# Optimization experiments

Hardware: AMD Instinct MI355X
Metric: run time of the kernel (lower is better)

## Reference

```python
import jax, jax.numpy as jnp
from jax import lax
import numpy as np

B, L, E, H, R, V = 64, 512, 256, 256, 50, 20000
NEG = 1e10  # seq_max_pool mask constant


def _conv1d(x, w, b):
    # x: (B, L, Cin) -> (B, L, Cout); kernel 3, 'same' padding (pad=1)
    y = lax.conv_general_dilated(x.transpose(0, 2, 1), w, (1,), [(1, 1)],
                                 dimension_numbers=('NCH', 'OIH', 'NCH'))
    return y.transpose(0, 2, 1) + b


def _lstm_step(x, h, c, W_ih, W_hh, b_ih, b_hh):
    # single-step LSTM, PyTorch gate order (i, f, g, o)
    gates = x @ W_ih.T + b_ih + h @ W_hh.T + b_hh
    i, f, g, o = jnp.split(gates, 4, axis=-1)
    c = jax.nn.sigmoid(f) * c + jax.nn.sigmoid(i) * jnp.tanh(g)
    h = jax.nn.sigmoid(o) * jnp.tanh(c)
    return h, c


def _attention(q, ctx, W_attn, b_attn):
    # Luong attention (IBM seq2seq style). q: (B,E), ctx: (B,L,E)
    scores = jnp.einsum('be,ble->bl', q, ctx)
    attn = jax.nn.softmax(scores, axis=-1)
    mix = jnp.einsum('bl,ble->be', attn, ctx)
    return jnp.tanh(jnp.concatenate([mix, q], axis=-1) @ W_attn.T + b_attn)


def setup_inputs() -> dict:
    key = jax.random.key(0)
    ks = jax.random.split(key, 25)
    s = 0.05
    return {
        'encoder_o': jax.random.normal(ks[0], (B, L, E), jnp.float32),
        'h0': jax.random.normal(ks[1], (B, H), jnp.float32),
        'c0': jax.random.normal(ks[2], (B, H), jnp.float32),
        'sos_emb': jax.random.normal(ks[3], (E,), jnp.float32) * s,
        'rel_emb': jax.random.normal(ks[4], (R, E), jnp.float32) * s,
        'W_ih': jax.random.normal(ks[5], (4 * H, E), jnp.float32) * s,
        'W_hh': jax.random.normal(ks[6], (4 * H, H), jnp.float32) * s,
        'b_ih': jax.random.normal(ks[7], (4 * H,), jnp.float32) * s,
        'b_hh': jax.random.normal(ks[8], (4 * H,), jnp.float32) * s,
        'W_attn': jax.random.normal(ks[9], (E, 2 * E), jnp.float32) * s,
        'b_attn': jax.random.normal(ks[10], (E,), jnp.float32) * s,
        'conv_rel_w': jax.random.normal(ks[11], (E, 2 * H, 3), jnp.float32) * s,
        'conv_rel_b': jax.random.normal(ks[12], (E,), jnp.float32) * s,
        'conv_ent_w': jax.random.normal(ks[13], (E, 2 * H, 3), jnp.float32) * s,
        'conv_ent_b': jax.random.normal(ks[14], (E,), jnp.float32) * s,
        'W_rel': jax.random.normal(ks[15], (R, E), jnp.float32) * s,
        'b_rel': jax.random.normal(ks[16], (R,), jnp.float32) * s,
        'w_e1': jax.random.normal(ks[17], (E,), jnp.float32) * s,
        'b_e1': jax.random.normal(ks[18], (1,), jnp.float32) * s,
        'w_e2': jax.random.normal(ks[19], (E,), jnp.float32) * s,
        'b_e2': jax.random.normal(ks[20], (1,), jnp.float32) * s,
        'T': jax.random.randint(ks[21], (B, L), 0, V),
        'R_in': jax.random.randint(ks[22], (B,), 0, R),
        'S_K1': jax.random.randint(ks[23], (B,), 0, L),
        'S_K2': jax.random.randint(ks[24], (B,), 0, L),
    }


def reference(encoder_o, h0, c0, sos_emb, rel_emb, W_ih, W_hh, b_ih, b_hh,
              W_attn, b_attn, conv_rel_w, conv_rel_b, conv_ent_w, conv_ent_b,
              W_rel, b_rel, w_e1, b_e1, w_e2, b_e2, T, R_in, S_K1, S_K2):
    # train_forward, order=('subject','predicate','object') -> sos2ent, ent2rel, rel2ent
    # dropout is identity (eval mode)
    mask = (T > 0).astype(encoder_o.dtype)[..., None]  # (B,L,1)
    bidx = jnp.arange(B)

    def step(inp, h, c, enc, conv_w, conv_b):
        # forward_step: one LSTM step + attention over enc
        h, c = _lstm_step(inp, h, c, W_ih, W_hh, b_ih, b_hh)
        out = _attention(h, enc, W_attn, b_attn)  # (B,E)
        # seq_and_vec + permute + conv1d + permute
        cat = jnp.concatenate([enc, jnp.broadcast_to(out[:, None, :], enc.shape)], axis=-1)
        new_enc = _conv1d(cat, conv_w, conv_b)  # (B,L,E)
        a = jax.nn.gelu(new_enc, approximate=False)
        return a, new_enc, h, c

    # step 1: sos -> entity heads
    a, enc1, h, c = step(jnp.broadcast_to(sos_emb, (B, E)), h0, c0, encoder_o,
                         conv_ent_w, conv_ent_b)
    t1e1 = a @ w_e1 + b_e1  # (B,L)
    t1e2 = a @ w_e2 + b_e2

    # step 2: gathered entity span vectors -> relation logits (masked max-pool)
    inp = enc1[bidx, S_K1] + enc1[bidx, S_K2]  # seq_gather + sum, (B,E)
    a, enc2, h, c = step(inp, h, c, enc1, conv_rel_w, conv_rel_b)
    logits = a @ W_rel.T + b_rel  # (B,L,R)
    t2rel = jnp.max(logits - (1.0 - mask) * NEG, axis=1)  # seq_max_pool -> (B,R)

    # step 3: relation embedding -> entity heads
    a, enc3, h, c = step(rel_emb[R_in], h, c, enc2, conv_ent_w, conv_ent_b)
    t3e1 = a @ w_e1 + b_e1
    t3e2 = a @ w_e2 + b_e2

    return (t1e1, t1e2, t2rel, t3e1, t3e2)
```

## Files before the change

### kernel.cpp

```cpp
#include <hip/hip_runtime.h>
#include <math.h>

#define B_ 64
#define L_ 512
#define E_ 256
#define H_ 256
#define R_ 50
#define NEG_ 1.0e10f

typedef __bf16 bf16x8 __attribute__((ext_vector_type(8)));
typedef float f32x4 __attribute__((ext_vector_type(4)));

__device__ __forceinline__ float sigmoidf_(float x) { return 1.0f / (1.0f + expf(-x)); }
__device__ __forceinline__ float geluf_(float x) { return 0.5f * x * (1.0f + erff(x * 0.7071067811865476f)); }
__device__ __forceinline__ unsigned short f2bf(float x) {
    unsigned u = __float_as_uint(x);
    return (unsigned short)((u + 0x7fffu + ((u >> 16) & 1u)) >> 16);
}
__device__ __forceinline__ float bf2f(unsigned u) { return __uint_as_float(u << 16); }

__global__ void k_packs(const float* __restrict__ encoder_o, unsigned short* __restrict__ encBF0,
                        const float* __restrict__ conv_ent_w, const float* __restrict__ conv_rel_w,
                        unsigned short* __restrict__ bpE, unsigned short* __restrict__ bpR,
                        const float* __restrict__ W_rel, unsigned short* __restrict__ wpR,
                        float* __restrict__ wpkE, float* __restrict__ wpkR,
                        const float* __restrict__ W_attn, float* __restrict__ WTat) {
    const int blk = blockIdx.x, t = threadIdx.x;
    if (blk < 8192) {
        size_t idx = (size_t)blk * 256 + t;
        float4 v = *(const float4*)&encoder_o[idx * 4];
        uint2 p;
        p.x = (unsigned)f2bf(v.x) | ((unsigned)f2bf(v.y) << 16);
        p.y = (unsigned)f2bf(v.z) | ((unsigned)f2bf(v.w) << 16);
        *(uint2*)&encBF0[idx * 4] = p;
    } else if (blk < 8384) {
        const float* w = (blk < 8288) ? conv_ent_w : conv_rel_w;
        unsigned short* bp = (blk < 8288) ? bpE : bpR;
        int idx = (blk - ((blk < 8288) ? 8192 : 8288)) * 256 + t;
        int l = idx & 63, kc = (idx >> 6) % 24, of = idx / (24 * 64);
        int o = of * 16 + (l & 15);
        int k = kc >> 3;
        int cb = ((kc & 7) << 5) + ((l >> 4) << 3);
        unsigned short v[8];
#pragma unroll
        for (int j = 0; j < 8; ++j) v[j] = f2bf(w[(size_t)o * 1536 + (size_t)(cb + j) * 3 + k]);
        unsigned int* dst = (unsigned int*)&bp[(size_t)idx * 8];
#pragma unroll
        for (int j = 0; j < 4; ++j) dst[j] = (unsigned int)v[2 * j] | ((unsigned int)v[2 * j + 1] << 16);
    } else if (blk < 8392) {
        int idx = (blk - 8384) * 256 + t;
        int l = idx & 63, kc = (idx >> 6) & 7, of = idx / (8 * 64);
        int r = of * 16 + (l & 15);
        int k = kc * 32 + ((l >> 4) << 3);
        unsigned short v[8];
#pragma unroll
        for (int j = 0; j < 8; ++j) v[j] = (r < R_) ? f2bf(W_rel[(size_t)r * E_ + k + j]) : 0;
        unsigned int* dst = (unsigned int*)&wpR[(size_t)idx * 8];
#pragma unroll
        for (int j = 0; j < 4; ++j) dst[j] = (unsigned int)v[2 * j] | ((unsigned int)v[2 * j + 1] << 16);
    } else if (blk < 8904) {
        const float* w = (blk < 8648) ? conv_ent_w : conv_rel_w;
        float* wpk = (blk < 8648) ? wpkE : wpkR;
        int idx = (blk - ((blk < 8648) ? 8392 : 8648)) * 256 + t;
        int o = idx >> 8, c = idx & 255;
        const float* p = &w[(size_t)o * 1536 + 768 + c * 3];
        float w0 = p[0], w1 = p[1], w2 = p[2];
        wpk[c * 256 + o] = w0;
        wpk[65536 + c * 256 + o] = w0 + w1 + w2;
        wpk[131072 + c * 256 + o] = w2;
    } else {
        int idx = (blk - 8904) * 256 + t;
        int o = idx >> 9, k = idx & 511;
        WTat[k * 256 + o] = W_attn[idx];
    }
}

template <int MODE>
__global__ __launch_bounds__(256) void k_lstm_gemm(
    const float* __restrict__ xsrc_f, const unsigned short* __restrict__ encg,
    const int* __restrict__ i1, const int* __restrict__ i2, const int* __restrict__ rin,
    const float* __restrict__ hprev,
    const float* __restrict__ W_ih, const float* __restrict__ W_hh,
    float* __restrict__ gates,
    const float* __restrict__ pmax, float* __restrict__ t2rel) {
    const int g0 = blockIdx.x * 64;
    const int half = blockIdx.y, z = blockIdx.z;
    const int t = threadIdx.x, tx = t & 15, ty = t >> 4;
    __shared__ float Xs[64][68];
    __shared__ float Wt[64][68];
    const float* Wsrc = half ? W_hh : W_ih;
    float acc[4][4] = {{0.f}};
    for (int kb = z * 128; kb < z * 128 + 128; kb += 64) {
        __syncthreads();
#pragma unroll
        for (int i = 0; i < 4; ++i) {
            int idx = i * 256 + t;
            int row = idx >> 4, kk = (idx & 15) << 2;
            float4 xv;
            if (half) {
                xv = *(const float4*)&hprev[row * 256 + kb + kk];
            } else if (MODE == 0) {
                xv = *(const float4*)&xsrc_f[kb + kk];
            } else if (MODE == 2) {
                xv = *(const float4*)&xsrc_f[(size_t)rin[row] * 256 + kb + kk];
            } else {
                const unsigned short* p1 = &encg[((size_t)row * L_ + i1[row]) * E_ + kb + kk];
                const unsigned short* p2 = &encg[((size_t)row * L_ + i2[row]) * E_ + kb + kk];
                uint2 a = *(const uint2*)p1, b2 = *(const uint2*)p2;
                xv.x = bf2f(a.x & 0xffffu) + bf2f(b2.x & 0xffffu);
                xv.y = bf2f(a.x >> 16) + bf2f(b2.x >> 16);
                xv.z = bf2f(a.y & 0xffffu) + bf2f(b2.y & 0xffffu);
                xv.w = bf2f(a.y >> 16) + bf2f(b2.y >> 16);
            }
            *(float4*)&Xs[row][kk] = xv;
            *(float4*)&Wt[row][kk] = *(const float4*)&Wsrc[(size_t)(g0 + row) * 256 + kb + kk];
        }
        __syncthreads();
#pragma unroll
        for (int kk = 0; kk < 64; kk += 4) {
            float4 xv[4], wv[4];
#pragma unroll
            for (int i = 0; i < 4; ++i) xv[i] = *(const float4*)&Xs[ty * 4 + i][kk];
#pragma unroll
            for (int j = 0; j < 4; ++j) wv[j] = *(const float4*)&Wt[tx * 4 + j][kk];
#pragma unroll
            for (int i = 0; i < 4; ++i)
#pragma unroll
                for (int j = 0; j < 4; ++j)
                    acc[i][j] += xv[i].x * wv[j].x + xv[i].y * wv[j].y + xv[i].z * wv[j].z + xv[i].w * wv[j].w;
        }
    }
    const int seg = half * 2 + z;
#pragma unroll
    for (int i = 0; i < 4; ++i)
#pragma unroll
        for (int j = 0; j < 4; ++j)
            gates[(size_t)seg * 65536 + (size_t)(ty * 4 + i) * 1024 + g0 + tx * 4 + j] = acc[i][j];

    if (MODE == 2 && blockIdx.x == 0 && half == 0 && z == 0) {
        for (int i = t; i < B_ * 64; i += 256) {
            int b = i >> 6, r = i & 63;
            if (r < R_) {
                float m = -3.0e38f;
#pragma unroll
                for (int ch = 0; ch < 8; ++ch) m = fmaxf(m, pmax[((size_t)b * 8 + ch) * 64 + r]);
                t2rel[b * R_ + r] = m;
            }
        }
    }
}

__global__ __launch_bounds__(256) void k_attn_part(
    const float* __restrict__ gates, const float* __restrict__ b_ih, const float* __restrict__ b_hh,
    const float* __restrict__ c_in, float* __restrict__ c_out, float* __restrict__ h_out,
    const unsigned short* __restrict__ encbf,
    float* __restrict__ mixp, float* __restrict__ stats) {
    int b = blockIdx.y, ch = blockIdx.x, t = threadIdx.x;
    __shared__ float hs[E_];
    __shared__ float scp[64][4];
    __shared__ float sc[64];
    {
        size_t ba = (size_t)b * 1024;
        float g4[4];
#pragma unroll
        for (int g = 0; g < 4; ++g) {
            float acc = b_ih[g * 256 + t] + b_hh[g * 256 + t];
#pragma unroll
            for (int seg = 0; seg < 4; ++seg) acc += gates[(size_t)seg * 65536 + ba + g * 256 + t];
            g4[g] = acc;
        }
        float c = sigmoidf_(g4[1]) * c_in[b * H_ + t] + sigmoidf_(g4[0]) * tanhf(g4[2]);
        float hv = sigmoidf_(g4[3]) * tanhf(c);
        hs[t] = hv;
        if (ch == 0) { h_out[b * H_ + t] = hv; c_out[b * H_ + t] = c; }
    }
    __syncthreads();
    {
        int row = t >> 2, es = t & 3;
        const uint4* p = (const uint4*)&encbf[((size_t)b * L_ + ch * 64 + row) * E_ + es * 64];
        float acc = 0.f;
#pragma unroll
        for (int k = 0; k < 8; ++k) {
            uint4 q = p[k];
            int e0 = es * 64 + k * 8;
            acc += bf2f(q.x & 0xffffu) * hs[e0] + bf2f(q.x >> 16) * hs[e0 + 1]
                 + bf2f(q.y & 0xffffu) * hs[e0 + 2] + bf2f(q.y >> 16) * hs[e0 + 3]
                 + bf2f(q.z & 0xffffu) * hs[e0 + 4] + bf2f(q.z >> 16) * hs[e0 + 5]
                 + bf2f(q.w & 0xffffu) * hs[e0 + 6] + bf2f(q.w >> 16) * hs[e0 + 7];
        }
        scp[row][es] = acc;
    }
    __syncthreads();
    if (t < 64) {
        float v = scp[t][0] + scp[t][1] + scp[t][2] + scp[t][3];
        float m = v;
#pragma unroll
        for (int off = 32; off; off >>= 1) m = fmaxf(m, __shfl_xor(m, off));
        float ev = expf(v - m);
        float s = ev;
#pragma unroll
        for (int off = 32; off; off >>= 1) s += __shfl_xor(s, off);
        sc[t] = ev;
        if (t == 0) {
            stats[((size_t)b * 8 + ch) * 2] = m;
            stats[((size_t)b * 8 + ch) * 2 + 1] = s;
        }
    }
    __syncthreads();
    float acc = 0.f;
    const unsigned short* base = &encbf[((size_t)b * L_ + ch * 64) * E_ + t];
#pragma unroll 8
    for (int l = 0; l < 64; ++l) acc += sc[l] * bf2f((unsigned)base[(size_t)l * E_]);
    mixp[((size_t)b * 8 + ch) * E_ + t] = acc;
}

__global__ __launch_bounds__(256) void k_post1(
    const float* __restrict__ mixp, const float* __restrict__ stats,
    const float* __restrict__ h, const float* __restrict__ WT_attn,
    const float* __restrict__ b_attn, float* __restrict__ aout) {
    int b = blockIdx.x, oc = blockIdx.y, t = threadIdx.x;
    __shared__ float cat[512];
    __shared__ float red[16][16][4];
    {
        float M = -3.0e38f;
#pragma unroll
        for (int i = 0; i < 8; ++i) M = fmaxf(M, stats[(b * 8 + i) * 2]);
        float denom = 0.f, mixv = 0.f;
#pragma unroll
        for (int i = 0; i < 8; ++i) {
            float w = expf(stats[(b * 8 + i) * 2] - M);
            denom += stats[(b * 8 + i) * 2 + 1] * w;
            mixv += mixp[((size_t)b * 8 + i) * E_ + t] * w;
        }
        cat[t] = mixv / denom;
        cat[256 + t] = h[b * H_ + t];
    }
    __syncthreads();
    int ocol = t & 15, ks = t >> 4;
    int o4 = oc * 64 + ocol * 4;
    float a0 = 0.f, a1 = 0.f, a2 = 0.f, a3 = 0.f;
    const float* wp = &WT_attn[(size_t)(ks * 32) * 256 + o4];
#pragma unroll 8
    for (int k = 0; k < 32; ++k) {
        float4 w = *(const float4*)&wp[(size_t)k * 256];
        float cv = cat[ks * 32 + k];
        a0 += cv * w.x; a1 += cv * w.y; a2 += cv * w.z; a3 += cv * w.w;
    }
    red[ks][ocol][0] = a0; red[ks][ocol][1] = a1; red[ks][ocol][2] = a2; red[ks][ocol][3] = a3;
    __syncthreads();
    if (t < 64) {
        int oc2 = t >> 2, j = t & 3;
        float s = 0.f;
#pragma unroll
        for (int k2 = 0; k2 < 16; ++k2) s += red[k2][oc2][j];
        int o = oc * 64 + t;
        aout[b * E_ + o] = tanhf(s + b_attn[o]);
    }
}

__global__ __launch_bounds__(256) void k_post2(
    const float* __restrict__ aout, const float* __restrict__ wpk,
    float* __restrict__ cr0, float* __restrict__ fullv, float* __restrict__ cr2) {
    int b = blockIdx.x, m = blockIdx.y, t = threadIdx.x;
    __shared__ float os[256];
    __shared__ float red[4][64][4];
    os[t] = aout[b * E_ + t];
    __syncthreads();
    int ocol = t & 63, cs = t >> 6;
    int o4 = ocol * 4;
    const float* wp = &wpk[(size_t)m * 65536 + (size_t)(cs * 64) * 256 + o4];
    float a0 = 0.f, a1 = 0.f, a2 = 0.f, a3 = 0.f;
#pragma unroll 8
    for (int c = 0; c < 64; ++c) {
        float4 w = *(const float4*)&wp[(size_t)c * 256];
        float v = os[cs * 64 + c];
        a0 += v * w.x; a1 += v * w.y; a2 += v * w.z; a3 += v * w.w;
    }
    red[cs][ocol][0] = a0; red[cs][ocol][1] = a1; red[cs][ocol][2] = a2; red[cs][ocol][3] = a3;
    __syncthreads();
    int oc2 = t >> 2, j = t & 3;
    float s = red[0][oc2][j] + red[1][oc2][j] + red[2][oc2][j] + red[3][oc2][j];
    float* dst = (m == 0) ? cr0 : (m == 1) ? fullv : cr2;
    dst[b * E_ + t] = s;
}

template <bool FUSE_HEADS, bool WRITE_OUT, bool FUSE_REL>
__global__ __launch_bounds__(512, 6) void k_conv_mfma(
    const unsigned short* __restrict__ encbf, const unsigned short* __restrict__ bp,
    const float* __restrict__ bias, const float* __restrict__ fullv,
    const float* __restrict__ cr0, const float* __restrict__ cr2,
    unsigned short* __restrict__ enc_out,
    const float* __restrict__ w_e1, const float* __restrict__ b_e1,
    const float* __restrict__ w_e2, const float* __restrict__ b_e2,
    float* __restrict__ o1, float* __restrict__ o2,
    const unsigned short* __restrict__ wprel, const float* __restrict__ b_rel,
    const int* __restrict__ T, float* __restrict__ pmax) {
    const int b = blockIdx.y, l0 = blockIdx.x * 64;
    const int t = threadIdx.x, lane = t & 63, wid = t >> 6;
    __shared__ unsigned short As[66 * 256];
    __shared__ float hsum[2][FUSE_HEADS ? 8 : 1][FUSE_HEADS ? 64 : 1];
    __shared__ float pm[FUSE_REL ? 8 : 1][2][16];
    __shared__ int Tm[FUSE_REL ? 64 : 1];

    if (FUSE_REL && t < 64) Tm[t] = T[b * L_ + l0 + t];

    for (int u = t; u < 66 * 32; u += 512) {
        int row = u >> 5, cu = u & 31;
        int l = l0 - 1 + row;
        uint4 v = {0u, 0u, 0u, 0u};
        if (l >= 0 && l < L_) v = *(const uint4*)&encbf[((size_t)b * L_ + l) * E_ + cu * 8];
        *(uint4*)&As[row * 256 + ((cu ^ (row & 7)) << 3)] = v;
    }
    __syncthreads();

    const int wo2 = wid * 2;
    f32x4 zero = {0.f, 0.f, 0.f, 0.f};
    f32x4 acc[4][2];
#pragma unroll
    for (int i = 0; i < 4; ++i) { acc[i][0] = zero; acc[i][1] = zero; }
    const int arow = lane & 15, agrp = lane >> 4;
    const unsigned short* bp0 = &bp[((size_t)wo2 * 24 * 64 + lane) * 8];
    const unsigned short* bp1 = &bp[((size_t)(wo2 + 1) * 24 * 64 + lane) * 8];

#pragma unroll 4
    for (int kc = 0; kc < 24; ++kc) {
        const int k = kc >> 3;
        const int g = ((kc & 7) << 2) + agrp;
        bf16x8 b0 = *(const bf16x8*)&bp0[(size_t)kc * 512];
        bf16x8 b1 = *(const bf16x8*)&bp1[(size_t)kc * 512];
#pragma unroll
        for (int mi = 0; mi < 4; ++mi) {
            int r = mi * 16 + arow + k;
            bf16x8 a = *(const bf16x8*)&As[r * 256 + ((g ^ (r & 7)) << 3)];
            acc[mi][0] = __builtin_amdgcn_mfma_f32_16x16x32_bf16(a, b0, acc[mi][0], 0, 0, 0);
            acc[mi][1] = __builtin_amdgcn_mfma_f32_16x16x32_bf16(a, b1, acc[mi][1], 0, 0, 0);
        }
    }

    float biasv[2], c0v[2], c2v[2], we1v[2], we2v[2];
#pragma unroll
    for (int ni = 0; ni < 2; ++ni) {
        int o = (wo2 + ni) * 16 + (lane & 15);
        biasv[ni] = bias[o] + fullv[b * E_ + o];
        c0v[ni] = cr0[b * E_ + o];
        c2v[ni] = cr2[b * E_ + o];
        if (FUSE_HEADS) { we1v[ni] = w_e1[o]; we2v[ni] = w_e2[o]; }
    }
    __syncthreads();

#pragma unroll
    for (int mi = 0; mi < 4; ++mi) {
#pragma unroll
        for (int r = 0; r < 4; ++r) {
            int lloc = mi * 16 + agrp * 4 + r;
            int lrow = l0 + lloc;
            float p1 = 0.f, p2 = 0.f;
#pragma unroll
            for (int ni = 0; ni < 2; ++ni) {
                int o = (wo2 + ni) * 16 + (lane & 15);
                float vv = acc[mi][ni][r] + biasv[ni];
                if (lrow == 0) vv -= c0v[ni];
                if (lrow == L_ - 1) vv -= c2v[ni];
                if (WRITE_OUT || FUSE_REL) {
                    int idx = FUSE_REL ? (lloc * 256 + ((((o >> 3) ^ (lloc & 7))) << 3) + (o & 7))
                                       : (lloc * 256 + o);
                    As[idx] = f2bf(vv);
                }
                if (FUSE_HEADS) {
                    float gv = geluf_(vv);
                    p1 += gv * we1v[ni];
                    p2 += gv * we2v[ni];
                }
            }
            if (FUSE_HEADS) {
#pragma unroll
                for (int off = 1; off < 16; off <<= 1) {
                    p1 += __shfl_xor(p1, off);
                    p2 += __shfl_xor(p2, off);
                }
                if ((lane & 15) == 0) {
                    hsum[0][wid][lloc] = p1;
                    hsum[1][wid][lloc] = p2;
                }
            }
        }
    }
    __syncthreads();

    if (WRITE_OUT) {
        for (int u = t; u < 64 * 32; u += 512) {
            int row = u >> 5, cu = u & 31;
            int src = FUSE_REL ? (row * 256 + ((cu ^ (row & 7)) << 3)) : (row * 256 + cu * 8);
            uint4 q = *(const uint4*)&As[src];
            *(uint4*)&enc_out[((size_t)b * L_ + l0 + row) * E_ + cu * 8] = q;
            if (FUSE_REL) {
                unsigned qa[4] = {q.x, q.y, q.z, q.w};
#pragma unroll
                for (int j = 0; j < 4; ++j) {
                    unsigned lo = f2bf(geluf_(bf2f(qa[j] & 0xffffu)));
                    unsigned hi = f2bf(geluf_(bf2f(qa[j] >> 16)));
                    qa[j] = lo | (hi << 16);
                }
                uint4 gq = {qa[0], qa[1], qa[2], qa[3]};
                *(uint4*)&As[src] = gq;
            }
        }
    }
    if (FUSE_HEADS && t < 128) {
        int hh = t >> 6, row = t & 63;
        float s = 0.f;
#pragma unroll
        for (int w = 0; w < 8; ++w) s += hsum[hh][w][row];
        float* dst = hh ? o2 : o1;
        const float* bb = hh ? b_e2 : b_e1;
        dst[(size_t)b * L_ + l0 + row] = s + bb[0];
    }
    if (FUSE_REL) {
        __syncthreads();
        const int mi = wid & 3, njp = wid >> 2;
        f32x4 accr[2] = {zero, zero};
        const int ar = mi * 16 + arow;
#pragma unroll 2
        for (int kc = 0; kc < 8; ++kc) {
            int g = (kc << 2) + agrp;
            bf16x8 av = *(const bf16x8*)&As[ar * 256 + ((g ^ (ar & 7)) << 3)];
#pragma unroll
            for (int q = 0; q < 2; ++q) {
                int nj = njp * 2 + q;
                bf16x8 bv = *(const bf16x8*)&wprel[(((size_t)nj * 8 + kc) * 64 + lane) * 8];
                accr[q] = __builtin_amdgcn_mfma_f32_16x16x32_bf16(av, bv, accr[q], 0, 0, 0);
            }
        }
#pragma unroll
        for (int q = 0; q < 2; ++q) {
            int nj = njp * 2 + q;
            int rr = nj * 16 + (lane & 15);
            float brel = (rr < R_) ? b_rel[rr] : 0.f;
            float v = -3.0e38f;
#pragma unroll
            for (int rg = 0; rg < 4; ++rg) {
                int lloc = mi * 16 + agrp * 4 + rg;
                float pen = (Tm[lloc] > 0) ? 0.f : NEG_;
                v = fmaxf(v, accr[q][rg] + brel - pen);
            }
            v = fmaxf(v, __shfl_xor(v, 16));
            v = fmaxf(v, __shfl_xor(v, 32));
            if (lane < 16) pm[wid][q][lane] = v;
        }
        __syncthreads();
        if (t < 64) {
            int nj = t >> 4, rl = t & 15;
            int q = nj & 1, wb = (nj >> 1) * 4;
            float m = fmaxf(fmaxf(pm[wb][q][rl], pm[wb + 1][q][rl]),
                            fmaxf(pm[wb + 2][q][rl], pm[wb + 3][q][rl]));
            pmax[((size_t)b * 8 + blockIdx.x) * 64 + t] = m;
        }
    }
}

extern "C" void kernel_launch(void* const* d_in, const int* in_sizes, int n_in,
                              void* d_out, int out_size, void* d_ws, size_t ws_size,
                              hipStream_t stream) {
    const float* encoder_o = (const float*)d_in[0];
    const float* h0 = (const float*)d_in[1];
    const float* c0 = (const float*)d_in[2];
    const float* sos_emb = (const float*)d_in[3];
    const float* rel_emb = (const float*)d_in[4];
    const float* W_ih = (const float*)d_in[5];
    const float* W_hh = (const float*)d_in[6];
    const float* b_ih = (const float*)d_in[7];
    const float* b_hh = (const float*)d_in[8];
    const float* W_attn = (const float*)d_in[9];
    const float* b_attn = (const float*)d_in[10];
    const float* conv_rel_w = (const float*)d_in[11];
    const float* conv_rel_b = (const float*)d_in[12];
    const float* conv_ent_w = (const float*)d_in[13];
    const float* conv_ent_b = (const float*)d_in[14];
    const float* W_rel = (const float*)d_in[15];
    const float* b_rel = (const float*)d_in[16];
    const float* w_e1 = (const float*)d_in[17];
    const float* b_e1 = (const float*)d_in[18];
    const float* w_e2 = (const float*)d_in[19];
    const float* b_e2 = (const float*)d_in[20];
    const int* T = (const int*)d_in[21];
    const int* R_in = (const int*)d_in[22];
    const int* S_K1 = (const int*)d_in[23];
    const int* S_K2 = (const int*)d_in[24];

    float* out = (float*)d_out;
    float* t1e1 = out;
    float* t1e2 = out + 32768;
    float* t2rel = out + 65536;
    float* t3e1 = out + 68736;
    float* t3e2 = out + 101504;

    float* ws = (float*)d_ws;
    size_t off = 0;
    unsigned short* encBF0 = (unsigned short*)(ws + off); off += (size_t)B_ * L_ * E_ / 2;
    unsigned short* encA = (unsigned short*)(ws + off); off += (size_t)B_ * L_ * E_ / 2;
    unsigned short* encB = (unsigned short*)(ws + off); off += (size_t)B_ * L_ * E_ / 2;
    float* gates = ws + off; off += 4 * 65536;
    float* hbuf = ws + off; off += B_ * H_;
    float* cb1 = ws + off; off += B_ * H_;
    float* cb2 = ws + off; off += B_ * H_;
    float* cb3 = ws + off; off += B_ * H_;
    float* mixp = ws + off; off += (size_t)B_ * 8 * E_;
    float* stats = ws + off; off += B_ * 8 * 2;
    float* aoutb = ws + off; off += B_ * E_;
    float* fullv = ws + off; off += B_ * E_;
    float* cr0 = ws + off; off += B_ * E_;
    float* cr2 = ws + off; off += B_ * E_;
    float* pmax = ws + off; off += B_ * 8 * 64;
    float* wpkE = ws + off; off += 3 * 65536;
    float* wpkR = ws + off; off += 3 * 65536;
    float* WTat = ws + off; off += 131072;
    unsigned short* bpE = (unsigned short*)(ws + off); off += 16 * 24 * 64 * 8 / 2;
    unsigned short* bpR = (unsigned short*)(ws + off); off += 16 * 24 * 64 * 8 / 2;
    unsigned short* wpR = (unsigned short*)(ws + off); off += 4 * 8 * 64 * 8 / 2;

    dim3 convGrid(8, B_);
    dim3 attnGrid(8, B_);
    dim3 lstmGrid(16, 2, 2);
    dim3 p1Grid(B_, 4);
    dim3 p2Grid(B_, 3);

    k_packs<<<9416, 256, 0, stream>>>(encoder_o, encBF0, conv_ent_w, conv_rel_w,
                                      bpE, bpR, W_rel, wpR, wpkE, wpkR, W_attn, WTat);

    k_lstm_gemm<0><<<lstmGrid, 256, 0, stream>>>(sos_emb, nullptr, nullptr, nullptr, nullptr,
                                                 h0, W_ih, W_hh, gates, nullptr, nullptr);
    k_attn_part<<<attnGrid, 256, 0, stream>>>(gates, b_ih, b_hh, c0, cb1, hbuf, encBF0, mixp, stats);
    k_post1<<<p1Grid, 256, 0, stream>>>(mixp, stats, hbuf, WTat, b_attn, aoutb);
    k_post2<<<p2Grid, 256, 0, stream>>>(aoutb, wpkE, cr0, fullv, cr2);
    k_conv_mfma<true, true, false><<<convGrid, 512, 0, stream>>>(
        encBF0, bpE, conv_ent_b, fullv, cr0, cr2, encA,
        w_e1, b_e1, w_e2, b_e2, t1e1, t1e2, nullptr, nullptr, nullptr, nullptr);

    k_lstm_gemm<1><<<lstmGrid, 256, 0, stream>>>(nullptr, encA, S_K1, S_K2, nullptr,
                                                 hbuf, W_ih, W_hh, gates, nullptr, nullptr);
    k_attn_part<<<attnGrid, 256, 0, stream>>>(gates, b_ih, b_hh, cb1, cb2, hbuf, encA, mixp, stats);
    k_post1<<<p1Grid, 256, 0, stream>>>(mixp, stats, hbuf, WTat, b_attn, aoutb);
    k_post2<<<p2Grid, 256, 0, stream>>>(aoutb, wpkR, cr0, fullv, cr2);
    k_conv_mfma<false, true, true><<<convGrid, 512, 0, stream>>>(
        encA, bpR, conv_rel_b, fullv, cr0, cr2, encB,
        nullptr, nullptr, nullptr, nullptr, nullptr, nullptr, wpR, b_rel, T, pmax);

    k_lstm_gemm<2><<<lstmGrid, 256, 0, stream>>>(rel_emb, nullptr, nullptr, nullptr, R_in,
                                                 hbuf, W_ih, W_hh, gates, pmax, t2rel);
    k_attn_part<<<attnGrid, 256, 0, stream>>>(gates, b_ih, b_hh, cb2, cb3, hbuf, encB, mixp, stats);
    k_post1<<<p1Grid, 256, 0, stream>>>(mixp, stats, hbuf, WTat, b_attn, aoutb);
    k_post2<<<p2Grid, 256, 0, stream>>>(aoutb, wpkE, cr0, fullv, cr2);
    k_conv_mfma<true, false, false><<<convGrid, 512, 0, stream>>>(
        encB, bpE, conv_ent_b, fullv, cr0, cr2, nullptr,
        w_e1, b_e1, w_e2, b_e2, t3e1, t3e2, nullptr, nullptr, nullptr, nullptr);
}
```

Before: 192.5 us.

## Fuse LSTM step, attention and conv-vector precompute into one per-batch kernel

Replaces the four per-step kernels (LSTM gate GEMM, partial attention, attention output projection, conv weight projection) with a single 1024-thread block per batch row that does all of them in shared memory. This removes three launches per step plus the global round trips for gates, partial mix and softmax stats. In exchange, each block re-reads the full W_ih/W_hh and attention/conv weights, so weight traffic grows by a factor of 64, and only 64 blocks run on the GPU. The conv kernel's launch-bounds occupancy hint is also lowered from 6 to 4.

```diff
diff --git a/kernel.cpp b/kernel.cpp
--- a/kernel.cpp
+++ b/kernel.cpp
@@ -76,113 +76,82 @@
 }
 
 template <int MODE>
-__global__ __launch_bounds__(256) void k_lstm_gemm(
+__global__ __launch_bounds__(1024) void k_mid(
     const float* __restrict__ xsrc_f, const unsigned short* __restrict__ encg,
     const int* __restrict__ i1, const int* __restrict__ i2, const int* __restrict__ rin,
-    const float* __restrict__ hprev,
+    const float* __restrict__ hprev, const float* __restrict__ c_in,
     const float* __restrict__ W_ih, const float* __restrict__ W_hh,
-    float* __restrict__ gates,
+    const float* __restrict__ b_ih, const float* __restrict__ b_hh,
+    const unsigned short* __restrict__ encbf,
+    const float* __restrict__ WTat, const float* __restrict__ b_attn,
+    const float* __restrict__ wpk,
+    float* __restrict__ h_out, float* __restrict__ c_out,
+    float* __restrict__ cr0, float* __restrict__ fullv, float* __restrict__ cr2,
     const float* __restrict__ pmax, float* __restrict__ t2rel) {
-    const int g0 = blockIdx.x * 64;
-    const int half = blockIdx.y, z = blockIdx.z;
-    const int t = threadIdx.x, tx = t & 15, ty = t >> 4;
-    __shared__ float Xs[64][68];
-    __shared__ float Wt[64][68];
-    const float* Wsrc = half ? W_hh : W_ih;
-    float acc[4][4] = {{0.f}};
-    for (int kb = z * 128; kb < z * 128 + 128; kb += 64) {
-        __syncthreads();
-#pragma unroll
-        for (int i = 0; i < 4; ++i) {
-            int idx = i * 256 + t;
-            int row = idx >> 4, kk = (idx & 15) << 2;
-            float4 xv;
-            if (half) {
-                xv = *(const float4*)&hprev[row * 256 + kb + kk];
-            } else if (MODE == 0) {
-                xv = *(const float4*)&xsrc_f[kb + kk];
-            } else if (MODE == 2) {
-                xv = *(const float4*)&xsrc_f[(size_t)rin[row] * 256 + kb + kk];
-            } else {
-                const unsigned short* p1 = &encg[((size_t)row * L_ + i1[row]) * E_ + kb + kk];
-                const unsigned short* p2 = &encg[((size_t)row * L_ + i2[row]) * E_ + kb + kk];
-                uint2 a = *(const uint2*)p1, b2 = *(const uint2*)p2;
-                xv.x = bf2f(a.x & 0xffffu) + bf2f(b2.x & 0xffffu);
-                xv.y = bf2f(a.x >> 16) + bf2f(b2.x >> 16);
-                xv.z = bf2f(a.y & 0xffffu) + bf2f(b2.y & 0xffffu);
-                xv.w = bf2f(a.y >> 16) + bf2f(b2.y >> 16);
-            }
-            *(float4*)&Xs[row][kk] = xv;
-            *(float4*)&Wt[row][kk] = *(const float4*)&Wsrc[(size_t)(g0 + row) * 256 + kb + kk];
-        }
-        __syncthreads();
-#pragma unroll
-        for (int kk = 0; kk < 64; kk += 4) {
-            float4 xv[4], wv[4];
-#pragma unroll
-            for (int i = 0; i < 4; ++i) xv[i] = *(const float4*)&Xs[ty * 4 + i][kk];
-#pragma unroll
-            for (int j = 0; j < 4; ++j) wv[j] = *(const float4*)&Wt[tx * 4 + j][kk];
-#pragma unroll
-            for (int i = 0; i < 4; ++i)
-#pragma unroll
-                for (int j = 0; j < 4; ++j)
-                    acc[i][j] += xv[i].x * wv[j].x + xv[i].y * wv[j].y + xv[i].z * wv[j].z + xv[i].w * wv[j].w;
-        }
-    }
-    const int seg = half * 2 + z;
-#pragma unroll
-    for (int i = 0; i < 4; ++i)
-#pragma unroll
-        for (int j = 0; j < 4; ++j)
-            gates[(size_t)seg * 65536 + (size_t)(ty * 4 + i) * 1024 + g0 + tx * 4 + j] = acc[i][j];
-
-    if (MODE == 2 && blockIdx.x == 0 && half == 0 && z == 0) {
-        for (int i = t; i < B_ * 64; i += 256) {
-            int b = i >> 6, r = i & 63;
-            if (r < R_) {
-                float m = -3.0e38f;
-#pragma unroll
-                for (int ch = 0; ch < 8; ++ch) m = fmaxf(m, pmax[((size_t)b * 8 + ch) * 64 + r]);
-                t2rel[b * R_ + r] = m;
-            }
-        }
-    }
-}
-
-__global__ __launch_bounds__(256) void k_attn_part(
-    const float* __restrict__ gates, const float* __restrict__ b_ih, const float* __restrict__ b_hh,
-    const float* __restrict__ c_in, float* __restrict__ c_out, float* __restrict__ h_out,
-    const unsigned short* __restrict__ encbf,
-    float* __restrict__ mixp, float* __restrict__ stats) {
-    int b = blockIdx.y, ch = blockIdx.x, t = threadIdx.x;
-    __shared__ float hs[E_];
-    __shared__ float scp[64][4];
-    __shared__ float sc[64];
+    const int b = blockIdx.x, t = threadIdx.x;
+    __shared__ float xs[512];
+    __shared__ float hs[256];
+    __shared__ float gt[1024];
+    __shared__ float scp[512][2];
+    __shared__ float sc[512];
+    __shared__ float red[16];
+    __shared__ float mixq[4][256];
+    __shared__ float cat[512];
+    __shared__ float redp[16][64][4];
+
+    if (MODE == 2 && t < R_) {
+        float m = -3.0e38f;
+#pragma unroll
+        for (int ch = 0; ch < 8; ++ch) m = fmaxf(m, pmax[((size_t)b * 8 + ch) * 64 + t]);
+        t2rel[b * R_ + t] = m;
+    }
+
+    if (t < 256) {
+        float xv;
+        if (MODE == 0) xv = xsrc_f[t];
+        else if (MODE == 2) xv = xsrc_f[(size_t)rin[b] * 256 + t];
+        else xv = bf2f((unsigned)encg[((size_t)b * L_ + i1[b]) * E_ + t]) +
+                  bf2f((unsigned)encg[((size_t)b * L_ + i2[b]) * E_ + t]);
+        xs[t] = xv;
+        xs[256 + t] = hprev[b * 256 + t];
+    }
+    __syncthreads();
+
     {
-        size_t ba = (size_t)b * 1024;
-        float g4[4];
-#pragma unroll
-        for (int g = 0; g < 4; ++g) {
-            float acc = b_ih[g * 256 + t] + b_hh[g * 256 + t];
-#pragma unroll
-            for (int seg = 0; seg < 4; ++seg) acc += gates[(size_t)seg * 65536 + ba + g * 256 + t];
-            g4[g] = acc;
-        }
-        float c = sigmoidf_(g4[1]) * c_in[b * H_ + t] + sigmoidf_(g4[0]) * tanhf(g4[2]);
-        float hv = sigmoidf_(g4[3]) * tanhf(c);
+        float acc = b_ih[t] + b_hh[t];
+        const float4* wi = (const float4*)&W_ih[(size_t)t * 256];
+        const float4* wh = (const float4*)&W_hh[(size_t)t * 256];
+#pragma unroll 8
+        for (int k = 0; k < 64; ++k) {
+            float4 a = wi[k];
+            acc += a.x * xs[4 * k] + a.y * xs[4 * k + 1] + a.z * xs[4 * k + 2] + a.w * xs[4 * k + 3];
+            float4 h4 = wh[k];
+            acc += h4.x * xs[256 + 4 * k] + h4.y * xs[256 + 4 * k + 1]
+                 + h4.z * xs[256 + 4 * k + 2] + h4.w * xs[256 + 4 * k + 3];
+        }
+        gt[t] = acc;
+    }
+    __syncthreads();
+
+    if (t < 256) {
+        float c = sigmoidf_(gt[256 + t]) * c_in[b * 256 + t] + sigmoidf_(gt[t]) * tanhf(gt[512 + t]);
+        float hv = sigmoidf_(gt[768 + t]) * tanhf(c);
         hs[t] = hv;
-        if (ch == 0) { h_out[b * H_ + t] = hv; c_out[b * H_ + t] = c; }
-    }
-    __syncthreads();
+        h_out[b * 256 + t] = hv;
+        c_out[b * 256 + t] = c;
+    }
+    __syncthreads();
+
     {
-        int row = t >> 2, es = t & 3;
-        const uint4* p = (const uint4*)&encbf[((size_t)b * L_ + ch * 64 + row) * E_ + es * 64];
+        int row = t >> 1, es = t & 1;
+        const uint4* pr = (const uint4*)&encg[0];
+        const uint4* p = (const uint4*)&encbf[((size_t)b * L_ + row) * E_ + es * 128];
+        (void)pr;
         float acc = 0.f;
 #pragma unroll
-        for (int k = 0; k < 8; ++k) {
+        for (int k = 0; k < 16; ++k) {
             uint4 q = p[k];
-            int e0 = es * 64 + k * 8;
+            int e0 = es * 128 + k * 8;
             acc += bf2f(q.x & 0xffffu) * hs[e0] + bf2f(q.x >> 16) * hs[e0 + 1]
                  + bf2f(q.y & 0xffffu) * hs[e0 + 2] + bf2f(q.y >> 16) * hs[e0 + 3]
                  + bf2f(q.z & 0xffffu) * hs[e0 + 4] + bf2f(q.z >> 16) * hs[e0 + 5]
@@ -191,101 +160,90 @@
         scp[row][es] = acc;
     }
     __syncthreads();
-    if (t < 64) {
-        float v = scp[t][0] + scp[t][1] + scp[t][2] + scp[t][3];
+
+    {
+        float v = (t < 512) ? (scp[t][0] + scp[t][1]) : -3.0e38f;
         float m = v;
 #pragma unroll
         for (int off = 32; off; off >>= 1) m = fmaxf(m, __shfl_xor(m, off));
-        float ev = expf(v - m);
+        if (t < 512 && (t & 63) == 0) red[t >> 6] = m;
+        __syncthreads();
+        float M = red[0];
+#pragma unroll
+        for (int i = 1; i < 8; ++i) M = fmaxf(M, red[i]);
+        float ev = (t < 512) ? expf(v - M) : 0.f;
         float s = ev;
 #pragma unroll
         for (int off = 32; off; off >>= 1) s += __shfl_xor(s, off);
-        sc[t] = ev;
-        if (t == 0) {
-            stats[((size_t)b * 8 + ch) * 2] = m;
-            stats[((size_t)b * 8 + ch) * 2 + 1] = s;
-        }
-    }
-    __syncthreads();
-    float acc = 0.f;
-    const unsigned short* base = &encbf[((size_t)b * L_ + ch * 64) * E_ + t];
+        if (t < 512 && (t & 63) == 0) red[8 + (t >> 6)] = s;
+        if (t < 512) sc[t] = ev;
+    }
+    __syncthreads();
+
+    {
+        int e = t & 255, q = t >> 8;
+        const unsigned short* base = &encbf[((size_t)b * L_ + q * 128) * E_ + e];
+        float acc = 0.f;
 #pragma unroll 8
-    for (int l = 0; l < 64; ++l) acc += sc[l] * bf2f((unsigned)base[(size_t)l * E_]);
-    mixp[((size_t)b * 8 + ch) * E_ + t] = acc;
-}
-
-__global__ __launch_bounds__(256) void k_post1(
-    const float* __restrict__ mixp, const float* __restrict__ stats,
-    const float* __restrict__ h, const float* __restrict__ WT_attn,
-    const float* __restrict__ b_attn, float* __restrict__ aout) {
-    int b = blockIdx.x, oc = blockIdx.y, t = threadIdx.x;
-    __shared__ float cat[512];
-    __shared__ float red[16][16][4];
+        for (int l = 0; l < 128; ++l) acc += sc[q * 128 + l] * bf2f((unsigned)base[(size_t)l * E_]);
+        mixq[q][e] = acc;
+    }
+    __syncthreads();
+
+    if (t < 256) {
+        float s = red[8] + red[9] + red[10] + red[11] + red[12] + red[13] + red[14] + red[15];
+        cat[t] = (mixq[0][t] + mixq[1][t] + mixq[2][t] + mixq[3][t]) / s;
+        cat[256 + t] = hs[t];
+    }
+    __syncthreads();
+
     {
-        float M = -3.0e38f;
-#pragma unroll
-        for (int i = 0; i < 8; ++i) M = fmaxf(M, stats[(b * 8 + i) * 2]);
-        float denom = 0.f, mixv = 0.f;
-#pragma unroll
-        for (int i = 0; i < 8; ++i) {
-            float w = expf(stats[(b * 8 + i) * 2] - M);
-            denom += stats[(b * 8 + i) * 2 + 1] * w;
-            mixv += mixp[((size_t)b * 8 + i) * E_ + t] * w;
-        }
-        cat[t] = mixv / denom;
-        cat[256 + t] = h[b * H_ + t];
-    }
-    __syncthreads();
-    int ocol = t & 15, ks = t >> 4;
-    int o4 = oc * 64 + ocol * 4;
-    float a0 = 0.f, a1 = 0.f, a2 = 0.f, a3 = 0.f;
-    const float* wp = &WT_attn[(size_t)(ks * 32) * 256 + o4];
+        int ocol = t & 63, ks = t >> 6;
+        float a0 = 0.f, a1 = 0.f, a2 = 0.f, a3 = 0.f;
+        const float* wp = &WTat[(size_t)(ks * 32) * 256 + ocol * 4];
 #pragma unroll 8
-    for (int k = 0; k < 32; ++k) {
-        float4 w = *(const float4*)&wp[(size_t)k * 256];
-        float cv = cat[ks * 32 + k];
-        a0 += cv * w.x; a1 += cv * w.y; a2 += cv * w.z; a3 += cv * w.w;
-    }
-    red[ks][ocol][0] = a0; red[ks][ocol][1] = a1; red[ks][ocol][2] = a2; red[ks][ocol][3] = a3;
-    __syncthreads();
-    if (t < 64) {
+        for (int k = 0; k < 32; ++k) {
+            float4 w = *(const float4*)&wp[(size_t)k * 256];
+            float cv = cat[ks * 32 + k];
+            a0 += cv * w.x; a1 += cv * w.y; a2 += cv * w.z; a3 += cv * w.w;
+        }
+        redp[ks][ocol][0] = a0; redp[ks][ocol][1] = a1;
+        redp[ks][ocol][2] = a2; redp[ks][ocol][3] = a3;
+    }
+    __syncthreads();
+    if (t < 256) {
         int oc2 = t >> 2, j = t & 3;
         float s = 0.f;
 #pragma unroll
-        for (int k2 = 0; k2 < 16; ++k2) s += red[k2][oc2][j];
-        int o = oc * 64 + t;
-        aout[b * E_ + o] = tanhf(s + b_attn[o]);
+        for (int k2 = 0; k2 < 16; ++k2) s += redp[k2][oc2][j];
+        hs[t] = tanhf(s + b_attn[t]);
+    }
+    __syncthreads();
+
+    {
+        float (*red2)[256] = (float(*)[256])gt;
+        for (int m = 0; m < 3; ++m) {
+            {
+                int o = t & 255, cs = t >> 8;
+                const float* wp = &wpk[(size_t)m * 65536 + (size_t)(cs * 64) * 256 + o];
+                float acc = 0.f;
+#pragma unroll 8
+                for (int c = 0; c < 64; ++c) acc += hs[cs * 64 + c] * wp[(size_t)c * 256];
+                red2[cs][o] = acc;
+            }
+            __syncthreads();
+            if (t < 256) {
+                float s = red2[0][t] + red2[1][t] + red2[2][t] + red2[3][t];
+                float* dst = (m == 0) ? cr0 : (m == 1) ? fullv : cr2;
+                dst[b * 256 + t] = s;
+            }
+            __syncthreads();
+        }
     }
 }
 
-__global__ __launch_bounds__(256) void k_post2(
-    const float* __restrict__ aout, const float* __restrict__ wpk,
-    float* __restrict__ cr0, float* __restrict__ fullv, float* __restrict__ cr2) {
-    int b = blockIdx.x, m = blockIdx.y, t = threadIdx.x;
-    __shared__ float os[256];
-    __shared__ float red[4][64][4];
-    os[t] = aout[b * E_ + t];
-    __syncthreads();
-    int ocol = t & 63, cs = t >> 6;
-    int o4 = ocol * 4;
-    const float* wp = &wpk[(size_t)m * 65536 + (size_t)(cs * 64) * 256 + o4];
-    float a0 = 0.f, a1 = 0.f, a2 = 0.f, a3 = 0.f;
-#pragma unroll 8
-    for (int c = 0; c < 64; ++c) {
-        float4 w = *(const float4*)&wp[(size_t)c * 256];
-        float v = os[cs * 64 + c];
-        a0 += v * w.x; a1 += v * w.y; a2 += v * w.z; a3 += v * w.w;
-    }
-    red[cs][ocol][0] = a0; red[cs][ocol][1] = a1; red[cs][ocol][2] = a2; red[cs][ocol][3] = a3;
-    __syncthreads();
-    int oc2 = t >> 2, j = t & 3;
-    float s = red[0][oc2][j] + red[1][oc2][j] + red[2][oc2][j] + red[3][oc2][j];
-    float* dst = (m == 0) ? cr0 : (m == 1) ? fullv : cr2;
-    dst[b * E_ + t] = s;
-}
-
 template <bool FUSE_HEADS, bool WRITE_OUT, bool FUSE_REL>
-__global__ __launch_bounds__(512, 6) void k_conv_mfma(
+__global__ __launch_bounds__(512, 4) void k_conv_mfma(
     const unsigned short* __restrict__ encbf, const unsigned short* __restrict__ bp,
     const float* __restrict__ bias, const float* __restrict__ fullv,
     const float* __restrict__ cr0, const float* __restrict__ cr2,
@@ -499,14 +457,12 @@
     unsigned short* encBF0 = (unsigned short*)(ws + off); off += (size_t)B_ * L_ * E_ / 2;
     unsigned short* encA = (unsigned short*)(ws + off); off += (size_t)B_ * L_ * E_ / 2;
     unsigned short* encB = (unsigned short*)(ws + off); off += (size_t)B_ * L_ * E_ / 2;
-    float* gates = ws + off; off += 4 * 65536;
-    float* hbuf = ws + off; off += B_ * H_;
+    float* hb1 = ws + off; off += B_ * H_;
+    float* hb2 = ws + off; off += B_ * H_;
+    float* hb3 = ws + off; off += B_ * H_;
     float* cb1 = ws + off; off += B_ * H_;
     float* cb2 = ws + off; off += B_ * H_;
     float* cb3 = ws + off; off += B_ * H_;
-    float* mixp = ws + off; off += (size_t)B_ * 8 * E_;
-    float* stats = ws + off; off += B_ * 8 * 2;
-    float* aoutb = ws + off; off += B_ * E_;
     float* fullv = ws + off; off += B_ * E_;
     float* cr0 = ws + off; off += B_ * E_;
     float* cr2 = ws + off; off += B_ * E_;
@@ -519,37 +475,30 @@
     unsigned short* wpR = (unsigned short*)(ws + off); off += 4 * 8 * 64 * 8 / 2;
 
     dim3 convGrid(8, B_);
-    dim3 attnGrid(8, B_);
-    dim3 lstmGrid(16, 2, 2);
-    dim3 p1Grid(B_, 4);
-    dim3 p2Grid(B_, 3);
 
     k_packs<<<9416, 256, 0, stream>>>(encoder_o, encBF0, conv_ent_w, conv_rel_w,
                                       bpE, bpR, W_rel, wpR, wpkE, wpkR, W_attn, WTat);
 
-    k_lstm_gemm<0><<<lstmGrid, 256, 0, stream>>>(sos_emb, nullptr, nullptr, nullptr, nullptr,
-                                                 h0, W_ih, W_hh, gates, nullptr, nullptr);
-    k_attn_part<<<attnGrid, 256, 0, stream>>>(gates, b_ih, b_hh, c0, cb1, hbuf, encBF0, mixp, stats);
-    k_post1<<<p1Grid, 256, 0, stream>>>(mixp, stats, hbuf, WTat, b_attn, aoutb);
-    k_post2<<<p2Grid, 256, 0, stream>>>(aoutb, wpkE, cr0, fullv, cr2);
+    k_mid<0><<<B_, 1024, 0, stream>>>(sos_emb, nullptr, nullptr, nullptr, nullptr,
+                                      h0, c0, W_ih, W_hh, b_ih, b_hh, encBF0,
+                                      WTat, b_attn, wpkE, hb1, cb1, cr0, fullv, cr2,
+                                      nullptr, nullptr);
     k_conv_mfma<true, true, false><<<convGrid, 512, 0, stream>>>(
         encBF0, bpE, conv_ent_b, fullv, cr0, cr2, encA,
         w_e1, b_e1, w_e2, b_e2, t1e1, t1e2, nullptr, nullptr, nullptr, nullptr);
 
-    k_lstm_gemm<1><<<lstmGrid, 256, 0, stream>>>(nullptr, encA, S_K1, S_K2, nullptr,
-                                                 hbuf, W_ih, W_hh, gates, nullptr, nullptr);
-    k_attn_part<<<attnGrid, 256, 0, stream>>>(gates, b_ih, b_hh, cb1, cb2, hbuf, encA, mixp, stats);
-    k_post1<<<p1Grid, 256, 0, stream>>>(mixp, stats, hbuf, WTat, b_attn, aoutb);
-    k_post2<<<p2Grid, 256, 0, stream>>>(aoutb, wpkR, cr0, fullv, cr2);
+    k_mid<1><<<B_, 1024, 0, stream>>>(nullptr, encA, S_K1, S_K2, nullptr,
+                                      hb1, cb1, W_ih, W_hh, b_ih, b_hh, encA,
+                                      WTat, b_attn, wpkR, hb2, cb2, cr0, fullv, cr2,
+                                      nullptr, nullptr);
     k_conv_mfma<false, true, true><<<convGrid, 512, 0, stream>>>(
         encA, bpR, conv_rel_b, fullv, cr0, cr2, encB,
         nullptr, nullptr, nullptr, nullptr, nullptr, nullptr, wpR, b_rel, T, pmax);
 
-    k_lstm_gemm<2><<<lstmGrid, 256, 0, stream>>>(rel_emb, nullptr, nullptr, nullptr, R_in,
-                                                 hbuf, W_ih, W_hh, gates, pmax, t2rel);
-    k_attn_part<<<attnGrid, 256, 0, stream>>>(gates, b_ih, b_hh, cb2, cb3, hbuf, encB, mixp, stats);
-    k_post1<<<p1Grid, 256, 0, stream>>>(mixp, stats, hbuf, WTat, b_attn, aoutb);
-    k_post2<<<p2Grid, 256, 0, stream>>>(aoutb, wpkE, cr0, fullv, cr2);
+    k_mid<2><<<B_, 1024, 0, stream>>>(rel_emb, nullptr, nullptr, nullptr, R_in,
+                                      hb2, cb2, W_ih, W_hh, b_ih, b_hh, encB,
+                                      WTat, b_attn, wpkE, hb3, cb3, cr0, fullv, cr2,
+                                      pmax, t2rel);
     k_conv_mfma<true, false, false><<<convGrid, 512, 0, stream>>>(
         encB, bpE, conv_ent_b, fullv, cr0, cr2, nullptr,
         w_e1, b_e1, w_e2, b_e2, t3e1, t3e2, nullptr, nullptr, nullptr, nullptr);
```

After: 358.7 us. 1.86x slower.
